# Performance work log

Measured on AMD Instinct MI355X. Metric: run time of the kernel, lower is better.

The kernel has to match this reference:

```python
import jax, jax.numpy as jnp
import numpy as np

DIM = 1024
HEADS = 16
HD = DIM // HEADS
EPS = 1e-5


def setup_inputs() -> dict:
    key = jax.random.key(0)
    ks = jax.random.split(key, 7)
    s = 0.02
    return {
        "x": jax.random.normal(ks[0], (2, 2048, DIM), dtype=jnp.float32),
        "w_qkv": jax.random.normal(ks[1], (DIM, 3 * DIM), dtype=jnp.float32) * s,
        "b_qkv": jnp.zeros((3 * DIM,), dtype=jnp.float32),
        "g_q": jnp.ones((HD,), dtype=jnp.float32),
        "be_q": jnp.zeros((HD,), dtype=jnp.float32),
        "g_k": jnp.ones((HD,), dtype=jnp.float32),
        "be_k": jnp.zeros((HD,), dtype=jnp.float32),
        "w_proj": jax.random.normal(ks[2], (DIM, DIM), dtype=jnp.float32) * s,
        "b_proj": jnp.zeros((DIM,), dtype=jnp.float32),
    }


def _ln(x, g, b):
    mu = jnp.mean(x, axis=-1, keepdims=True)
    var = jnp.var(x, axis=-1, keepdims=True)
    return (x - mu) * jax.lax.rsqrt(var + EPS) * g + b


def reference(x, w_qkv, b_qkv, g_q, be_q, g_k, be_k, w_proj, b_proj):
    B, N, C = x.shape
    qkv = x @ w_qkv + b_qkv                      # [B,N,3C]
    qkv = qkv.reshape(B, N, 3, HEADS, HD).transpose(2, 0, 3, 1, 4)  # [3,B,H,N,hd]
    q, k, v = qkv[0], qkv[1], qkv[2]
    q = _ln(q, g_q, be_q) * (HD ** -0.5)
    k = _ln(k, g_k, be_k)
    attn = jax.nn.softmax(jnp.einsum("bhqd,bhkd->bhqk", q, k), axis=-1)
    out = jnp.einsum("bhqk,bhkd->bhqd", attn, v)  # [B,H,N,hd]
    out = out.transpose(0, 2, 1, 3).reshape(B, N, C)
    return out @ w_proj + b_proj
```

## Files before the change

kernel.cpp:

```cpp
#include <hip/hip_runtime.h>


typedef short bf16x8 __attribute__((ext_vector_type(8)));
typedef float f32x4  __attribute__((ext_vector_type(4)));

__device__ __forceinline__ short f2bf(float f) {
  union { float f; unsigned u; } c; c.f = f;
  unsigned r = c.u + 0x7fffu + ((c.u >> 16) & 1u);
  return (short)(r >> 16);
}

__device__ __forceinline__ void gld16(const void* g, void* l) {
  __builtin_amdgcn_global_load_lds(
      (const __attribute__((address_space(1))) unsigned int*)(unsigned long long)g,
      (__attribute__((address_space(3))) unsigned int*)(unsigned int)(unsigned long long)l,
      16, 0, 0);
}

__global__ void k_cvt(const float* __restrict__ in, short* __restrict__ out, int n) {
  int i = (blockIdx.x * blockDim.x + threadIdx.x) * 4;
  if (i < n) {
    float4 f = *(const float4*)(in + i);
    short4 s;
    s.x = f2bf(f.x); s.y = f2bf(f.y); s.z = f2bf(f.z); s.w = f2bf(f.w);
    *(short4*)(out + i) = s;
  }
}

__global__ void k_transpose(const float* __restrict__ in, short* __restrict__ out,
                            int R, int C) {
  __shared__ float t[32][33];
  const int tx = threadIdx.x, ty = threadIdx.y;
  const int c0 = blockIdx.x * 32, r0 = blockIdx.y * 32;
#pragma unroll
  for (int i = 0; i < 4; i++)
    t[ty * 4 + i][tx] = in[(size_t)(r0 + ty * 4 + i) * C + c0 + tx];
  __syncthreads();
#pragma unroll
  for (int i = 0; i < 4; i++)
    out[(size_t)(c0 + ty * 4 + i) * R + r0 + tx] = f2bf(t[tx][ty * 4 + i]);
}

__device__ __forceinline__ void mm_loop(const short* __restrict__ A,
                                        const short* __restrict__ B,
                                        int K, int mBase, int nBase,
                                        short* As, short* Bs, f32x4 acc[4][4]) {
  const int tid = threadIdx.x;
  const int w = tid >> 6, lane = tid & 63;
  const int wr = w >> 1, wc = w & 1;
  const int lhi = lane >> 4, llo = lane & 15;
  const int rin = lane >> 3;
  const int kin = (lane & 7) * 8;

  const f32x4 fz = {0.f, 0.f, 0.f, 0.f};
#pragma unroll
  for (int mi = 0; mi < 4; mi++)
#pragma unroll
    for (int ni = 0; ni < 4; ni++) acc[mi][ni] = fz;

  const int nkt = K >> 6;
  for (int kb = 0; kb < nkt; kb++) {
    const int k0 = kb << 6;
#pragma unroll
    for (int i = 0; i < 4; i++) {
      const int c = w * 4 + i;
      const int row = c * 8 + rin;
      gld16(A + (size_t)(mBase + row) * K + k0 + kin, As + c * 512);
      gld16(B + (size_t)(nBase + row) * K + k0 + kin, Bs + c * 512);
    }
    __syncthreads();
#pragma unroll
    for (int kk = 0; kk < 2; kk++) {
      bf16x8 a[4], b[4];
#pragma unroll
      for (int mi = 0; mi < 4; mi++)
        a[mi] = *(const bf16x8*)(As + (wr * 64 + mi * 16 + llo) * 64 + kk * 32 + lhi * 8);
#pragma unroll
      for (int ni = 0; ni < 4; ni++)
        b[ni] = *(const bf16x8*)(Bs + (wc * 64 + ni * 16 + llo) * 64 + kk * 32 + lhi * 8);
#pragma unroll
      for (int mi = 0; mi < 4; mi++)
#pragma unroll
        for (int ni = 0; ni < 4; ni++)
          acc[mi][ni] = __builtin_amdgcn_mfma_f32_16x16x32_bf16(a[mi], b[ni], acc[mi][ni], 0, 0, 0);
    }
    __syncthreads();
  }
}

__global__ __launch_bounds__(256) void k_gemm_qkv(
    const short* __restrict__ A, const short* __restrict__ B,
    const float* __restrict__ bqkv,
    const float* __restrict__ g_q, const float* __restrict__ be_q,
    const float* __restrict__ g_k, const float* __restrict__ be_k,
    short* __restrict__ Qg, short* __restrict__ Kg, short* __restrict__ Vtg) {
  __shared__ short As[128 * 64];
  __shared__ short Bs[128 * 64];
  f32x4 acc[4][4];
  const int mBase = blockIdx.x * 128, nBase = blockIdx.y * 128;
  mm_loop(A, B, 1024, mBase, nBase, As, Bs, acc);

  const int tid = threadIdx.x;
  const int w = tid >> 6, lane = tid & 63;
  const int wr = w >> 1, wc = w & 1;
  const int lhi = lane >> 4, llo = lane & 15;

  const int cg0 = nBase + wc * 64;
  const int t = cg0 >> 10;
  const int h = (cg0 & 1023) >> 6;

  float bias[4], gg[4], bb[4];
#pragma unroll
  for (int ni = 0; ni < 4; ni++) {
    const int d = ni * 16 + llo;
    bias[ni] = bqkv[cg0 + d];
    if (t == 0)      { gg[ni] = g_q[d]; bb[ni] = be_q[d]; }
    else if (t == 1) { gg[ni] = g_k[d]; bb[ni] = be_k[d]; }
    else             { gg[ni] = 1.f;    bb[ni] = 0.f; }
  }

#pragma unroll
  for (int mi = 0; mi < 4; mi++) {
    float v[4][4];
#pragma unroll
    for (int ni = 0; ni < 4; ni++)
#pragma unroll
      for (int j = 0; j < 4; j++) v[ni][j] = acc[mi][ni][j] + bias[ni];

    if (t < 2) {
#pragma unroll
      for (int j = 0; j < 4; j++) {
        float s = 0.f, s2 = 0.f;
#pragma unroll
        for (int ni = 0; ni < 4; ni++) { s += v[ni][j]; s2 += v[ni][j] * v[ni][j]; }
#pragma unroll
        for (int msk = 1; msk < 16; msk <<= 1) {
          s  += __shfl_xor(s,  msk, 64);
          s2 += __shfl_xor(s2, msk, 64);
        }
        const float mu = s * 0.015625f;
        const float var = s2 * 0.015625f - mu * mu;
        const float rs = rsqrtf(var + 1e-5f);
#pragma unroll
        for (int ni = 0; ni < 4; ni++) {
          float y = (v[ni][j] - mu) * rs * gg[ni] + bb[ni];
          if (t == 0) y *= 0.125f;
          v[ni][j] = y;
        }
      }
    }
    const int rbase = mBase + wr * 64 + mi * 16 + lhi * 4;
#pragma unroll
    for (int j = 0; j < 4; j++) {
      const int r = rbase + j;
      const int b_ = r >> 11;
      const int n = r & 2047;
      const int bh = b_ * 16 + h;
#pragma unroll
      for (int ni = 0; ni < 4; ni++) {
        const int d = ni * 16 + llo;
        const short val = f2bf(v[ni][j]);
        if (t == 0)      Qg[((size_t)bh * 2048 + n) * 64 + d] = val;
        else if (t == 1) Kg[((size_t)bh * 2048 + n) * 64 + d] = val;
        else             Vtg[((size_t)bh * 64 + d) * 2048 + n] = val;
      }
    }
  }
}

__global__ __launch_bounds__(256) void k_attn(const short* __restrict__ Qg,
                                              const short* __restrict__ Kg,
                                              const short* __restrict__ Vtg,
                                              short* __restrict__ aout) {
  __shared__ short Ks[2][4096];
  __shared__ short Vs[2][4096];
  __shared__ short Ps[4][1024];
  const int tid = threadIdx.x;
  const int w = tid >> 6, lane = tid & 63;
  const int lhi = lane >> 4, llo = lane & 15;
  const int rin = lane >> 3;
  const int tg = (lane & 7) ^ rin;
  const int bh = blockIdx.y;
  const int qrow0 = blockIdx.x * 64 + w * 16;

  const short* Qrow = Qg + ((size_t)bh * 2048 + qrow0 + llo) * 64;
  const bf16x8 qa0 = *(const bf16x8*)(Qrow + lhi * 8);
  const bf16x8 qa1 = *(const bf16x8*)(Qrow + 32 + lhi * 8);

  bf16x8 onesb;
#pragma unroll
  for (int e = 0; e < 8; e++) onesb[e] = (short)0x3F80;

  const f32x4 fz = {0.f, 0.f, 0.f, 0.f};
  f32x4 o[4];
#pragma unroll
  for (int dg = 0; dg < 4; dg++) o[dg] = fz;
  f32x4 lsum = fz;

  short* Pw = Ps[w];
  const size_t kbase = (size_t)bh * 2048;
  const size_t vbase = (size_t)bh * 64;

#define STAGE(buf, kt_)                                                        \
  {                                                                            \
    const int kr0_ = (kt_) * 64;                                               \
    _Pragma("unroll")                                                          \
    for (int i = 0; i < 4; i++) {                                              \
      const int cc = w * 4 + i;                                                \
      if (cc < 8) {                                                            \
        gld16(Kg + (kbase + kr0_ + cc * 8 + rin) * 64 + tg * 8,                \
              &Ks[buf][cc * 512]);                                             \
      } else {                                                                 \
        const int c2 = cc - 8;                                                 \
        gld16(Vtg + (vbase + c2 * 8 + rin) * 2048 + kr0_ + tg * 8,             \
              &Vs[buf][c2 * 512]);                                             \
      }                                                                        \
    }                                                                          \
  }

  STAGE(0, 0);
  __syncthreads();
  int cur = 0;

  for (int kt = 0; kt < 32; kt++) {
    if (kt < 31) STAGE(cur ^ 1, kt + 1);

    const short* Kc = Ks[cur];
    const short* Vc = Vs[cur];

    f32x4 s[4];
#pragma unroll
    for (int krg = 0; krg < 4; krg++) {
      const int rk = krg * 16 + llo;
      const int sw = rk & 7;
      const bf16x8 kb0 = *(const bf16x8*)(Kc + rk * 64 + ((lhi ^ sw)) * 8);
      const bf16x8 kb1 = *(const bf16x8*)(Kc + rk * 64 + (((4 + lhi) ^ sw)) * 8);
      f32x4 z = fz;
      z = __builtin_amdgcn_mfma_f32_16x16x32_bf16(qa0, kb0, z, 0, 0, 0);
      z = __builtin_amdgcn_mfma_f32_16x16x32_bf16(qa1, kb1, z, 0, 0, 0);
      s[krg] = z;
    }

#pragma unroll
    for (int krg = 0; krg < 4; krg++)
#pragma unroll
      for (int j = 0; j < 4; j++) {
        const float p = __expf(s[krg][j]);
        const int row = lhi * 4 + j;
        const int slot = (krg * 2 + (llo >> 3)) ^ (row & 7);
        Pw[row * 64 + slot * 8 + (llo & 7)] = f2bf(p);
      }

    const int swp = llo & 7;
    const bf16x8 pa0 = *(const bf16x8*)(Pw + llo * 64 + ((lhi ^ swp)) * 8);
    const bf16x8 pa1 = *(const bf16x8*)(Pw + llo * 64 + (((4 + lhi) ^ swp)) * 8);

    lsum = __builtin_amdgcn_mfma_f32_16x16x32_bf16(pa0, onesb, lsum, 0, 0, 0);
    lsum = __builtin_amdgcn_mfma_f32_16x16x32_bf16(pa1, onesb, lsum, 0, 0, 0);

#pragma unroll
    for (int dg = 0; dg < 4; dg++) {
      const int rv = dg * 16 + llo;
      const int swv = rv & 7;
      const bf16x8 vb0 = *(const bf16x8*)(Vc + rv * 64 + ((lhi ^ swv)) * 8);
      const bf16x8 vb1 = *(const bf16x8*)(Vc + rv * 64 + (((4 + lhi) ^ swv)) * 8);
      o[dg] = __builtin_amdgcn_mfma_f32_16x16x32_bf16(pa0, vb0, o[dg], 0, 0, 0);
      o[dg] = __builtin_amdgcn_mfma_f32_16x16x32_bf16(pa1, vb1, o[dg], 0, 0, 0);
    }
    __syncthreads();
    cur ^= 1;
  }
#undef STAGE

  const int b_ = bh >> 4, h = bh & 15;
#pragma unroll
  for (int j = 0; j < 4; j++) {
    const float inv = 1.f / lsum[j];
    const int n = qrow0 + lhi * 4 + j;
#pragma unroll
    for (int dg = 0; dg < 4; dg++)
      aout[((size_t)(b_ * 2048 + n)) * 1024 + h * 64 + dg * 16 + llo] = f2bf(o[dg][j] * inv);
  }
}

__global__ __launch_bounds__(256) void k_gemm_proj(const short* __restrict__ A,
                                                   const short* __restrict__ B,
                                                   const float* __restrict__ bias,
                                                   float* __restrict__ C) {
  __shared__ short As[128 * 64];
  __shared__ short Bs[128 * 64];
  f32x4 acc[4][4];
  const int mBase = blockIdx.x * 128, nBase = blockIdx.y * 128;
  mm_loop(A, B, 1024, mBase, nBase, As, Bs, acc);

  const int tid = threadIdx.x;
  const int w = tid >> 6, lane = tid & 63;
  const int wr = w >> 1, wc = w & 1;
  const int lhi = lane >> 4, llo = lane & 15;
#pragma unroll
  for (int mi = 0; mi < 4; mi++)
#pragma unroll
    for (int ni = 0; ni < 4; ni++) {
      const int col = nBase + wc * 64 + ni * 16 + llo;
      const float bv = bias[col];
#pragma unroll
      for (int j = 0; j < 4; j++) {
        const int row = mBase + wr * 64 + mi * 16 + lhi * 4 + j;
        C[(size_t)row * 1024 + col] = acc[mi][ni][j] + bv;
      }
    }
}

extern "C" void kernel_launch(void* const* d_in, const int* in_sizes, int n_in,
                              void* d_out, int out_size, void* d_ws, size_t ws_size,
                              hipStream_t stream) {
  const float* x      = (const float*)d_in[0];
  const float* w_qkv  = (const float*)d_in[1];
  const float* b_qkv  = (const float*)d_in[2];
  const float* g_q    = (const float*)d_in[3];
  const float* be_q   = (const float*)d_in[4];
  const float* g_k    = (const float*)d_in[5];
  const float* be_k   = (const float*)d_in[6];
  const float* w_proj = (const float*)d_in[7];
  const float* b_proj = (const float*)d_in[8];
  float* out = (float*)d_out;

  char* ws = (char*)d_ws;
  short* xb     = (short*)(ws);
  short* wqkvT  = (short*)(ws + ((size_t)8  << 20));
  short* wprojT = (short*)(ws + ((size_t)14 << 20));
  short* Qg     = (short*)(ws + ((size_t)16 << 20));
  short* Kg     = (short*)(ws + ((size_t)24 << 20));
  short* Vtg    = (short*)(ws + ((size_t)32 << 20));
  short* aout   = (short*)(ws + ((size_t)40 << 20));

  k_cvt<<<4096, 256, 0, stream>>>(x, xb, 4096 * 1024);
  k_transpose<<<dim3(3072 / 32, 1024 / 32), dim3(32, 8), 0, stream>>>(w_qkv, wqkvT, 1024, 3072);
  k_transpose<<<dim3(1024 / 32, 1024 / 32), dim3(32, 8), 0, stream>>>(w_proj, wprojT, 1024, 1024);
  k_gemm_qkv<<<dim3(32, 24), 256, 0, stream>>>(xb, wqkvT, b_qkv, g_q, be_q, g_k, be_k, Qg, Kg, Vtg);
  k_attn<<<dim3(32, 32), 256, 0, stream>>>(Qg, Kg, Vtg, aout);
  k_gemm_proj<<<dim3(32, 8), 256, 0, stream>>>(aout, wprojT, b_proj, out);
}
```

Measured before the change: 234.5 us.

## Double-buffer GEMM LDS tiles and vectorize attention P stores with priority hints

The shared GEMM main loop now double-buffers its A/B LDS tiles, prefetching the next K slice with async global-to-LDS loads while MFMAs run on the current one. This hides load latency at the cost of twice the LDS per block (64KB), which may lower occupancy. In the attention kernel the QK^T MFMA operands are swapped so each lane holds four consecutive keys, letting P be packed and written with one 8-byte store instead of scalar 2-byte stores. s_setprio hints are added around the MFMA sections to favour matrix work across waves.

```diff
diff --git a/kernel.cpp b/kernel.cpp
--- a/kernel.cpp
+++ b/kernel.cpp
@@ -59,25 +59,36 @@
     for (int ni = 0; ni < 4; ni++) acc[mi][ni] = fz;
 
   const int nkt = K >> 6;
+
+#define MMSTAGE(buf, kb_)                                                      \
+  {                                                                            \
+    const int k0_ = (kb_) << 6;                                                \
+    _Pragma("unroll")                                                          \
+    for (int i = 0; i < 4; i++) {                                              \
+      const int c = w * 4 + i;                                                 \
+      const int row = c * 8 + rin;                                             \
+      gld16(A + (size_t)(mBase + row) * K + k0_ + kin, As + (buf) * 8192 + c * 512); \
+      gld16(B + (size_t)(nBase + row) * K + k0_ + kin, Bs + (buf) * 8192 + c * 512); \
+    }                                                                          \
+  }
+
+  MMSTAGE(0, 0);
+  __syncthreads();
+  int cur = 0;
+
   for (int kb = 0; kb < nkt; kb++) {
-    const int k0 = kb << 6;
-#pragma unroll
-    for (int i = 0; i < 4; i++) {
-      const int c = w * 4 + i;
-      const int row = c * 8 + rin;
-      gld16(A + (size_t)(mBase + row) * K + k0 + kin, As + c * 512);
-      gld16(B + (size_t)(nBase + row) * K + k0 + kin, Bs + c * 512);
-    }
-    __syncthreads();
+    if (kb + 1 < nkt) MMSTAGE(cur ^ 1, kb + 1);
+    const short* Ac = As + cur * 8192;
+    const short* Bc = Bs + cur * 8192;
 #pragma unroll
     for (int kk = 0; kk < 2; kk++) {
       bf16x8 a[4], b[4];
 #pragma unroll
       for (int mi = 0; mi < 4; mi++)
-        a[mi] = *(const bf16x8*)(As + (wr * 64 + mi * 16 + llo) * 64 + kk * 32 + lhi * 8);
+        a[mi] = *(const bf16x8*)(Ac + (wr * 64 + mi * 16 + llo) * 64 + kk * 32 + lhi * 8);
 #pragma unroll
       for (int ni = 0; ni < 4; ni++)
-        b[ni] = *(const bf16x8*)(Bs + (wc * 64 + ni * 16 + llo) * 64 + kk * 32 + lhi * 8);
+        b[ni] = *(const bf16x8*)(Bc + (wc * 64 + ni * 16 + llo) * 64 + kk * 32 + lhi * 8);
 #pragma unroll
       for (int mi = 0; mi < 4; mi++)
 #pragma unroll
@@ -85,7 +96,9 @@
           acc[mi][ni] = __builtin_amdgcn_mfma_f32_16x16x32_bf16(a[mi], b[ni], acc[mi][ni], 0, 0, 0);
     }
     __syncthreads();
-  }
+    cur ^= 1;
+  }
+#undef MMSTAGE
 }
 
 __global__ __launch_bounds__(256) void k_gemm_qkv(
@@ -94,8 +107,8 @@
     const float* __restrict__ g_q, const float* __restrict__ be_q,
     const float* __restrict__ g_k, const float* __restrict__ be_k,
     short* __restrict__ Qg, short* __restrict__ Kg, short* __restrict__ Vtg) {
-  __shared__ short As[128 * 64];
-  __shared__ short Bs[128 * 64];
+  __shared__ short As[2 * 8192];
+  __shared__ short Bs[2 * 8192];
   f32x4 acc[4][4];
   const int mBase = blockIdx.x * 128, nBase = blockIdx.y * 128;
   mm_loop(A, B, 1024, mBase, nBase, As, Bs, acc);
@@ -229,6 +242,7 @@
     const short* Vc = Vs[cur];
 
     f32x4 s[4];
+    __builtin_amdgcn_s_setprio(1);
 #pragma unroll
     for (int krg = 0; krg < 4; krg++) {
       const int rk = krg * 16 + llo;
@@ -236,25 +250,32 @@
       const bf16x8 kb0 = *(const bf16x8*)(Kc + rk * 64 + ((lhi ^ sw)) * 8);
       const bf16x8 kb1 = *(const bf16x8*)(Kc + rk * 64 + (((4 + lhi) ^ sw)) * 8);
       f32x4 z = fz;
-      z = __builtin_amdgcn_mfma_f32_16x16x32_bf16(qa0, kb0, z, 0, 0, 0);
-      z = __builtin_amdgcn_mfma_f32_16x16x32_bf16(qa1, kb1, z, 0, 0, 0);
+      z = __builtin_amdgcn_mfma_f32_16x16x32_bf16(kb0, qa0, z, 0, 0, 0);
+      z = __builtin_amdgcn_mfma_f32_16x16x32_bf16(kb1, qa1, z, 0, 0, 0);
       s[krg] = z;
     }
-
-#pragma unroll
-    for (int krg = 0; krg < 4; krg++)
-#pragma unroll
-      for (int j = 0; j < 4; j++) {
-        const float p = __expf(s[krg][j]);
-        const int row = lhi * 4 + j;
-        const int slot = (krg * 2 + (llo >> 3)) ^ (row & 7);
-        Pw[row * 64 + slot * 8 + (llo & 7)] = f2bf(p);
-      }
+    __builtin_amdgcn_s_setprio(0);
+
+#pragma unroll
+    for (int krg = 0; krg < 4; krg++) {
+      const float p0 = __expf(s[krg][0]);
+      const float p1 = __expf(s[krg][1]);
+      const float p2 = __expf(s[krg][2]);
+      const float p3 = __expf(s[krg][3]);
+      const unsigned u0 = (unsigned)(unsigned short)f2bf(p0) |
+                          ((unsigned)(unsigned short)f2bf(p1) << 16);
+      const unsigned u1 = (unsigned)(unsigned short)f2bf(p2) |
+                          ((unsigned)(unsigned short)f2bf(p3) << 16);
+      char* pb = (char*)Pw + llo * 128 +
+                 (((krg * 2 + (lhi >> 1)) ^ (llo & 7)) << 4) + ((lhi & 1) << 3);
+      *(uint2*)pb = make_uint2(u0, u1);
+    }
 
     const int swp = llo & 7;
     const bf16x8 pa0 = *(const bf16x8*)(Pw + llo * 64 + ((lhi ^ swp)) * 8);
     const bf16x8 pa1 = *(const bf16x8*)(Pw + llo * 64 + (((4 + lhi) ^ swp)) * 8);
 
+    __builtin_amdgcn_s_setprio(1);
     lsum = __builtin_amdgcn_mfma_f32_16x16x32_bf16(pa0, onesb, lsum, 0, 0, 0);
     lsum = __builtin_amdgcn_mfma_f32_16x16x32_bf16(pa1, onesb, lsum, 0, 0, 0);
 
@@ -267,6 +288,7 @@
       o[dg] = __builtin_amdgcn_mfma_f32_16x16x32_bf16(pa0, vb0, o[dg], 0, 0, 0);
       o[dg] = __builtin_amdgcn_mfma_f32_16x16x32_bf16(pa1, vb1, o[dg], 0, 0, 0);
     }
+    __builtin_amdgcn_s_setprio(0);
     __syncthreads();
     cur ^= 1;
   }
@@ -287,8 +309,8 @@
                                                    const short* __restrict__ B,
                                                    const float* __restrict__ bias,
                                                    float* __restrict__ C) {
-  __shared__ short As[128 * 64];
-  __shared__ short Bs[128 * 64];
+  __shared__ short As[2 * 8192];
+  __shared__ short Bs[2 * 8192];
   f32x4 acc[4][4];
   const int mBase = blockIdx.x * 128, nBase = blockIdx.y * 128;
   mm_loop(A, B, 1024, mBase, nBase, As, Bs, acc);
```

Measured after the change: 220.1 us. 1.07x faster.
